# Optimization experiments

Measured on AMD Instinct MI355X. Metric: run time of the kernel, lower is better.

Reference implementation:

```python
import jax, jax.numpy as jnp
import numpy as np

H, W = 256, 256          # resolution from __init__ default
FLOW_SCALING = 256.0     # max(resolution)
MAX_TS = 1.0             # events timestamps normalized to [0, 1]
EPS = 1e-9


def _warp_event(events, flow, tref, ts_weights=None):
    """Bilinear splatting of motion-compensated events into per-polarity IWE.
    events: [B,N,4] (ts,x,y,p); flow: [B,N,2]. Returns [B,2,H,W]."""
    ts = events[..., 0]                      # [B,N]
    x = events[..., 1]
    y = events[..., 2]
    pol = events[..., 3]
    # warped (floating-point) positions
    wx = x + (tref - ts) * flow[..., 0] * FLOW_SCALING
    wy = y + (tref - ts) * flow[..., 1] * FLOW_SCALING
    lx = jnp.floor(wx)
    ty = jnp.floor(wy)
    # 4 bilinear corners: [B,4,N]
    cx = jnp.stack([lx, lx + 1.0, lx, lx + 1.0], axis=1)
    cy = jnp.stack([ty, ty, ty + 1.0, ty + 1.0], axis=1)
    w = (jnp.maximum(0.0, 1.0 - jnp.abs(wx[:, None, :] - cx))
         * jnp.maximum(0.0, 1.0 - jnp.abs(wy[:, None, :] - cy)))
    inb = (cx >= 0) & (cx <= W - 1) & (cy >= 0) & (cy <= H - 1)
    w = jnp.where(inb, w, 0.0)
    if ts_weights is not None:               # optional per-event weight (ts)
        w = w * ts_weights[:, None, :]
    flat = (jnp.clip(cy, 0, H - 1) * W + jnp.clip(cx, 0, W - 1)).astype(jnp.int32)

    def splat(f, ww):  # scatter-add one batch element into flat H*W histogram
        return jnp.zeros(H * W, dtype=w.dtype).at[f.reshape(-1)].add(ww.reshape(-1))

    pos_w = jnp.where((pol == 1)[:, None, :], w, 0.0)
    neg_w = jnp.where((pol == -1)[:, None, :], w, 0.0)
    iwe_pos = jax.vmap(splat)(flat, pos_w).reshape(-1, H, W)
    iwe_neg = jax.vmap(splat)(flat, neg_w).reshape(-1, H, W)
    return jnp.stack([iwe_pos, iwe_neg], axis=1)  # [B,2,H,W]


def _warp_contrast(tref, flow, events):
    iwe = _warp_event(events, flow, tref)
    ts_iwe = _warp_event(events, flow, tref, ts_weights=events[..., 0])
    ts_iwe = ts_iwe / (iwe + EPS)
    loss = (ts_iwe ** 2).sum(axis=(1, 2, 3))           # [B]
    non_zero = ((iwe[:, 0] + iwe[:, 1]) > 0).astype(iwe.dtype)
    return loss / non_zero.sum(axis=(1, 2))


def setup_inputs() -> dict:
    key = jax.random.key(0)
    k1, k2, k3, k4, k5 = jax.random.split(key, 5)
    B, N = 2, 1_000_000
    ts = jax.random.uniform(k1, (B, N))
    x = jax.random.uniform(k2, (B, N)) * (W - 1)
    y = jax.random.uniform(k3, (B, N)) * (H - 1)
    p = jnp.where(jax.random.bernoulli(k4, 0.5, (B, N)), 1.0, -1.0)
    events = jnp.stack([ts, x, y, p], axis=-1).astype(jnp.float32)  # [B,N,4]
    flow = (jax.random.normal(k5, (B, N, 2)) * 0.05).astype(jnp.float32)
    return {"events": events, "flow": flow}


def reference(events, flow):
    # temporal contrast-maximization loss: forward + backward warp per pass
    fw = _warp_contrast(MAX_TS, flow, events).sum() / MAX_TS ** 2
    bw = _warp_contrast(0.0, flow, events).sum() / MAX_TS ** 2
    return fw + bw
```

## Files before the change

### kernel.cpp

```cpp
#include <hip/hip_runtime.h>

#define HH 256
#define WW 256
#define HW (HH * WW)
#define BATCH 2
#define NPASS 2
#define EPSF 1e-9f
#define FLOW_SCALE 256.0f

#define NBLK1 512
#define NCH 4
#define SCAP 1280
#define CAP 4288
#define FPSCALE 16777216.0f
#define FPINV (1.0f / 16777216.0f)

__global__ __launch_bounds__(256) void ew_bin8(
    const float4* __restrict__ events, const float2* __restrict__ flow,
    float* __restrict__ recs, unsigned* __restrict__ tbl, int N) {
  const int b = blockIdx.y;
  const int gblk = b * NBLK1 + blockIdx.x;
  events += (size_t)b * N;
  flow += (size_t)b * N;
  const int EB = (N + NBLK1 - 1) / NBLK1;
  const int i0 = blockIdx.x * EB;
  const int iend = (i0 + EB < N) ? i0 + EB : N;
  const int CEB = (EB + NCH - 1) / NCH;

  __shared__ float stage[SCAP * 3];
  __shared__ unsigned cnt[128], scan[128], start[128], cur[128];
  __shared__ unsigned s_base;
  if (threadIdx.x == 0) s_base = 0u;

  float* __restrict__ myrecs = recs + (size_t)gblk * CAP * 3;

  for (int c = 0; c < NCH; ++c) {
    const int j0 = i0 + c * CEB;
    int j1 = j0 + CEB;
    if (j1 > iend) j1 = iend;
    if (threadIdx.x < 128) {
      cnt[threadIdx.x] = 0u;
      cur[threadIdx.x] = 0u;
    }
    __syncthreads();

    for (int i = j0 + threadIdx.x; i < j1; i += 256) {
      const float4 e = events[i];
      const float2 f = flow[i];
#pragma unroll
      for (int pass = 0; pass < 2; ++pass) {
        const float tref = (pass == 0) ? 1.0f : 0.0f;
        const float dt = tref - e.x;
        const float wx = fmaf(dt * f.x, FLOW_SCALE, e.y);
        const float wy = fmaf(dt * f.y, FLOW_SCALE, e.z);
        const int lx = (int)floorf(wx), ly = (int)floorf(wy);
        int txs[2], tys[2], nx = 0, ny = 0;
        if ((unsigned)lx < 256u) txs[nx++] = lx >> 5;
        if ((unsigned)(lx + 1) < 256u &&
            (lx < 0 || (((lx + 1) >> 5) != (lx >> 5))))
          txs[nx++] = (lx + 1) >> 5;
        if ((unsigned)ly < 256u) tys[ny++] = ly >> 5;
        if ((unsigned)(ly + 1) < 256u &&
            (ly < 0 || (((ly + 1) >> 5) != (ly >> 5))))
          tys[ny++] = (ly + 1) >> 5;
        for (int a = 0; a < ny; ++a)
          for (int c2 = 0; c2 < nx; ++c2)
            atomicAdd(&cnt[pass * 64 + tys[a] * 8 + txs[c2]], 1u);
      }
    }
    __syncthreads();

    if (threadIdx.x < 64) {
      const int l = threadIdx.x;
      unsigned a = cnt[l], bq = cnt[64 + l];
      for (int off = 1; off < 64; off <<= 1) {
        const unsigned ta = __shfl_up(a, off, 64);
        const unsigned tb = __shfl_up(bq, off, 64);
        if (l >= off) {
          a += ta;
          bq += tb;
        }
      }
      const unsigned tot0 = __shfl(a, 63, 64);
      scan[l] = a;
      scan[64 + l] = bq + tot0;
    }
    __syncthreads();

    const unsigned base = s_base;
    unsigned total = scan[127];
    if (total > SCAP) total = SCAP;
    if (total > CAP - base) total = CAP - base;
    if (threadIdx.x < 128) {
      const unsigned c0 = cnt[threadIdx.x];
      const unsigned st = scan[threadIdx.x] - c0;
      unsigned ec = 0u;
      if (st < total) ec = (c0 < total - st) ? c0 : (total - st);
      start[threadIdx.x] = st;
      tbl[((size_t)gblk * 128 + threadIdx.x) * NCH + c] =
          (base + st) | (ec << 16);
    }
    __syncthreads();

    for (int i = j0 + threadIdx.x; i < j1; i += 256) {
      const float4 e = events[i];
      const float2 f = flow[i];
      const float tsp = copysignf(e.x, e.w);
#pragma unroll
      for (int pass = 0; pass < 2; ++pass) {
        const float tref = (pass == 0) ? 1.0f : 0.0f;
        const float dt = tref - e.x;
        const float wx = fmaf(dt * f.x, FLOW_SCALE, e.y);
        const float wy = fmaf(dt * f.y, FLOW_SCALE, e.z);
        const int lx = (int)floorf(wx), ly = (int)floorf(wy);
        int txs[2], tys[2], nx = 0, ny = 0;
        if ((unsigned)lx < 256u) txs[nx++] = lx >> 5;
        if ((unsigned)(lx + 1) < 256u &&
            (lx < 0 || (((lx + 1) >> 5) != (lx >> 5))))
          txs[nx++] = (lx + 1) >> 5;
        if ((unsigned)ly < 256u) tys[ny++] = ly >> 5;
        if ((unsigned)(ly + 1) < 256u &&
            (ly < 0 || (((ly + 1) >> 5) != (ly >> 5))))
          tys[ny++] = (ly + 1) >> 5;
        for (int a = 0; a < ny; ++a)
          for (int c2 = 0; c2 < nx; ++c2) {
            const int bin = pass * 64 + tys[a] * 8 + txs[c2];
            const unsigned pos = start[bin] + atomicAdd(&cur[bin], 1u);
            if (pos < total) {
              stage[pos * 3 + 0] = wx;
              stage[pos * 3 + 1] = wy;
              stage[pos * 3 + 2] = tsp;
            }
          }
      }
    }
    __syncthreads();

    const unsigned nf = total * 3;
    float* __restrict__ dst = myrecs + (size_t)base * 3;
    for (unsigned j = threadIdx.x; j < nf; j += 256) dst[j] = stage[j];
    __syncthreads();
    if (threadIdx.x == 0) s_base = base + total;
  }
}

__global__ __launch_bounds__(512) void ew_accum9(
    const float* __restrict__ recs, const uint4* __restrict__ tbl4,
    unsigned long long* __restrict__ histU, int nrep) {
  const int gbin = blockIdx.x;
  const int rep = blockIdx.y;
  const int b = gbin >> 7;
  const int bin127 = gbin & 127;
  const int pass = (gbin >> 6) & 1;
  const int tile = gbin & 63;
  const int tx0 = (tile & 7) * 32;
  const int ty0 = (tile >> 3) * 32;
  const int pb = pass * 2 + b;

  __shared__ unsigned long long lds64[2048];
  for (int j = threadIdx.x; j < 2048; j += 512) lds64[j] = 0ull;
  __syncthreads();

  const int bpr = NBLK1 / nrep;
  const int blk0 = rep * bpr;
  const int grp = threadIdx.x >> 3;
  const int lane = threadIdx.x & 7;
  for (int r = blk0 + grp; r < blk0 + bpr; r += 64) {
    const int gblk = b * NBLK1 + r;
    const float* __restrict__ blkrec = recs + (size_t)gblk * CAP * 3;
    const uint4 tv = tbl4[(size_t)gblk * 128 + bin127];
    const unsigned tvs[4] = {tv.x, tv.y, tv.z, tv.w};
#pragma unroll
    for (int c = 0; c < NCH; ++c) {
      const unsigned st = tvs[c] & 0xffffu;
      const unsigned ct = tvs[c] >> 16;
      for (unsigned k = lane; k < ct; k += 8) {
        const float wx = blkrec[(st + k) * 3 + 0];
        const float wy = blkrec[(st + k) * 3 + 1];
        const unsigned tb = __float_as_uint(blkrec[(st + k) * 3 + 2]);
        const int spol = (int)(tb >> 31);
        const float ts = __uint_as_float(tb & 0x7fffffffu);
        const int lx = (int)floorf(wx), ly = (int)floorf(wy);
        const float fx = wx - (float)lx;
        const float fy = wy - (float)ly;
        const float wxs[2] = {1.0f - fx, fx};
        const float wys[2] = {1.0f - fy, fy};
#pragma unroll
        for (int dy = 0; dy < 2; ++dy) {
          const int lcy = ly + dy - ty0;
          if ((unsigned)lcy >= 32u) continue;
#pragma unroll
          for (int dx = 0; dx < 2; ++dx) {
            const int lcx = lx + dx - tx0;
            if ((unsigned)lcx >= 32u) continue;
            const float w = wxs[dx] * wys[dy];
            const unsigned wq = __float2uint_rn(w * FPSCALE);
            const unsigned tq = __float2uint_rn(w * ts * FPSCALE);
            const unsigned long long v =
                ((unsigned long long)wq << 32) | (unsigned long long)tq;
            atomicAdd(&lds64[spol * 1024 + lcy * 32 + lcx], v);
          }
        }
      }
    }
  }
  __syncthreads();

  for (int j = threadIdx.x; j < 2048; j += 512) {
    const int spol = j >> 10;
    const int within = j & 1023;
    const size_t px = (size_t)(ty0 + (within >> 5)) * WW + tx0 + (within & 31);
    histU[(((size_t)rep * 4 + pb) * 2 + spol) * HW + px] = lds64[j];
  }
}

__global__ __launch_bounds__(256) void ew_reduce6(
    const unsigned long long* __restrict__ histU, float* __restrict__ partial,
    int nrep) {
  const int sub = blockIdx.x;
  const int pb = blockIdx.y;
  float loss = 0.0f, nz = 0.0f;
  for (int k = threadIdx.x; k < 2048; k += 256) {
    const int pix = sub * 2048 + k;
    unsigned long long v0 = 0ull, v1 = 0ull;
    for (int r = 0; r < nrep; ++r) {
      v0 += histU[(((size_t)r * 4 + pb) * 2 + 0) * HW + pix];
      v1 += histU[(((size_t)r * 4 + pb) * 2 + 1) * HW + pix];
    }
    const float ip = (float)(unsigned)(v0 >> 32) * FPINV;
    const float tp = (float)(unsigned)(v0 & 0xffffffffull) * FPINV;
    const float in_ = (float)(unsigned)(v1 >> 32) * FPINV;
    const float tn = (float)(unsigned)(v1 & 0xffffffffull) * FPINV;
    const float a = tp / (ip + EPSF);
    const float d = tn / (in_ + EPSF);
    loss += a * a + d * d;
    nz += ((ip + in_) > 0.0f) ? 1.0f : 0.0f;
  }
  for (int off = 32; off > 0; off >>= 1) {
    loss += __shfl_down(loss, off, 64);
    nz += __shfl_down(nz, off, 64);
  }
  __shared__ float sl[4], sn[4];
  const int wid = threadIdx.x >> 6;
  if ((threadIdx.x & 63) == 0) {
    sl[wid] = loss;
    sn[wid] = nz;
  }
  __syncthreads();
  if (threadIdx.x == 0) {
    partial[pb * 32 + sub] = sl[0] + sl[1] + sl[2] + sl[3];
    partial[128 + pb * 32 + sub] = sn[0] + sn[1] + sn[2] + sn[3];
  }
}

__global__ void ew_final2(const float* __restrict__ partial,
                          float* __restrict__ out) {
  if (threadIdx.x == 0 && blockIdx.x == 0) {
    float s = 0.0f;
    for (int pb = 0; pb < 4; ++pb) {
      float L = 0.0f, Z = 0.0f;
      for (int j = 0; j < 32; ++j) {
        L += partial[pb * 32 + j];
        Z += partial[128 + pb * 32 + j];
      }
      s += L / Z;
    }
    out[0] = s;
  }
}

#define CHUNKS 8
#define TILES 16
#define TILE_PX 4096
#define REP_FLOATS (CHUNKS * 16 * HW)

__global__ __launch_bounds__(256) void ew_tile(
    const float4* __restrict__ events, const float2* __restrict__ flow,
    float* __restrict__ rep, int N) {
  const int c = blockIdx.x;
  const int tile = blockIdx.y;
  const int pb = blockIdx.z;
  const int b = pb & 1;
  const float tref = (pb >> 1) == 0 ? 1.0f : 0.0f;
  const int tx0 = (tile & 3) * 64;
  const int ty0 = (tile >> 2) * 64;

  __shared__ float lds[4 * TILE_PX];
  for (int j = threadIdx.x; j < 4 * TILE_PX; j += 256) lds[j] = 0.0f;
  __syncthreads();

  events += (size_t)b * N;
  flow += (size_t)b * N;
  const int Nc = (N + CHUNKS - 1) / CHUNKS;
  const int i0 = c * Nc;
  const int i1 = (i0 + Nc < N) ? (i0 + Nc) : N;

  for (int i = i0 + threadIdx.x; i < i1; i += 256) {
    const float4 e = events[i];
    const float2 f = flow[i];
    const float ts = e.x;
    const int pol = (e.w > 0.0f) ? 0 : 1;
    const float dt = tref - ts;
    const float wx = fmaf(dt * f.x, FLOW_SCALE, e.y);
    const float wy = fmaf(dt * f.y, FLOW_SCALE, e.z);
    const float lxf = floorf(wx);
    const float tyf = floorf(wy);
    const float fx = wx - lxf;
    const float fy = wy - tyf;
    const int lx = (int)lxf - tx0;
    const int ty = (int)tyf - ty0;
    const float wxs[2] = {1.0f - fx, fx};
    const float wys[2] = {1.0f - fy, fy};
#pragma unroll
    for (int dy = 0; dy < 2; ++dy) {
      const int cy = ty + dy;
      if ((unsigned)cy >= 64u) continue;
#pragma unroll
      for (int dx = 0; dx < 2; ++dx) {
        const int cx = lx + dx;
        if ((unsigned)cx >= 64u) continue;
        const float w = wxs[dx] * wys[dy];
        const int li = cy * 64 + cx;
        atomicAdd(&lds[pol * TILE_PX + li], w);
        atomicAdd(&lds[(pol + 2) * TILE_PX + li], w * ts);
      }
    }
  }
  __syncthreads();

  float* __restrict__ dst = rep + ((size_t)c * 16 + (size_t)pb * 4) * HW;
  for (int j = threadIdx.x; j < 4 * TILE_PX; j += 256) {
    const int slice = j >> 12;
    const int within = j & (TILE_PX - 1);
    dst[(size_t)slice * HW + (ty0 + (within >> 6)) * WW + tx0 + (within & 63)] =
        lds[j];
  }
}

__global__ __launch_bounds__(256) void ew_reduce2(const float* __restrict__ rep,
                                                  float* __restrict__ partial) {
  const int sub = blockIdx.x;
  const int pb = blockIdx.y;
  float loss = 0.0f, nz = 0.0f;
  for (int k = threadIdx.x; k < 2048; k += 256) {
    const int pix = sub * 2048 + k;
    float ip = 0.0f, in_ = 0.0f, tp = 0.0f, tn = 0.0f;
#pragma unroll
    for (int c = 0; c < CHUNKS; ++c) {
      const float* __restrict__ rb =
          rep + ((size_t)c * 16 + (size_t)pb * 4) * HW + pix;
      ip += rb[0];
      in_ += rb[HW];
      tp += rb[2 * HW];
      tn += rb[3 * HW];
    }
    const float a = tp / (ip + EPSF);
    const float d = tn / (in_ + EPSF);
    loss += a * a + d * d;
    nz += ((ip + in_) > 0.0f) ? 1.0f : 0.0f;
  }
  for (int off = 32; off > 0; off >>= 1) {
    loss += __shfl_down(loss, off, 64);
    nz += __shfl_down(nz, off, 64);
  }
  __shared__ float sl[4], sn[4];
  const int wid = threadIdx.x >> 6;
  if ((threadIdx.x & 63) == 0) {
    sl[wid] = loss;
    sn[wid] = nz;
  }
  __syncthreads();
  if (threadIdx.x == 0) {
    partial[pb * 32 + sub] = sl[0] + sl[1] + sl[2] + sl[3];
    partial[128 + pb * 32 + sub] = sn[0] + sn[1] + sn[2] + sn[3];
  }
}

#define HIST_FLOATS (NPASS * BATCH * 4 * HW)

__global__ __launch_bounds__(256) void ew_scatter(
    const float4* __restrict__ events, const float2* __restrict__ flow,
    float* __restrict__ hist, int N) {
  const int b = blockIdx.y;
  events += (size_t)b * N;
  flow += (size_t)b * N;
  float* __restrict__ hb = hist + (size_t)b * 4 * HW;
  for (int i = blockIdx.x * blockDim.x + threadIdx.x; i < N;
       i += gridDim.x * blockDim.x) {
    const float4 e = events[i];
    const float2 f = flow[i];
    const float ts = e.x, x = e.y, y = e.z, p = e.w;
    const int polofs = (p > 0.0f) ? 0 : HW;
#pragma unroll
    for (int pass = 0; pass < NPASS; ++pass) {
      const float tref = (pass == 0) ? 1.0f : 0.0f;
      const float dt = tref - ts;
      const float wx = fmaf(dt * f.x, FLOW_SCALE, x);
      const float wy = fmaf(dt * f.y, FLOW_SCALE, y);
      const float lxf = floorf(wx), tyf = floorf(wy);
      const float fx = wx - lxf, fy = wy - tyf;
      const int lx = (int)lxf, ty = (int)tyf;
      float* __restrict__ wbase = hb + (size_t)pass * BATCH * 4 * HW + polofs;
      float* __restrict__ tbase = wbase + 2 * HW;
      const float w00 = (1.0f - fx) * (1.0f - fy);
      const float w10 = fx * (1.0f - fy);
      const float w01 = (1.0f - fx) * fy;
      const float w11 = fx * fy;
      const int cx0 = lx, cx1 = lx + 1, cy0 = ty, cy1 = ty + 1;
      const bool inx0 = (cx0 >= 0) & (cx0 < WW);
      const bool inx1 = (cx1 >= 0) & (cx1 < WW);
      const bool iny0 = (cy0 >= 0) & (cy0 < HH);
      const bool iny1 = (cy1 >= 0) & (cy1 < HH);
      if (inx0 & iny0) {
        const int pix = cy0 * WW + cx0;
        atomicAdd(wbase + pix, w00);
        atomicAdd(tbase + pix, w00 * ts);
      }
      if (inx1 & iny0) {
        const int pix = cy0 * WW + cx1;
        atomicAdd(wbase + pix, w10);
        atomicAdd(tbase + pix, w10 * ts);
      }
      if (inx0 & iny1) {
        const int pix = cy1 * WW + cx0;
        atomicAdd(wbase + pix, w01);
        atomicAdd(tbase + pix, w01 * ts);
      }
      if (inx1 & iny1) {
        const int pix = cy1 * WW + cx1;
        atomicAdd(wbase + pix, w11);
        atomicAdd(tbase + pix, w11 * ts);
      }
    }
  }
}

__global__ __launch_bounds__(256) void ew_reduce(const float* __restrict__ hist,
                                                 float* __restrict__ partial) {
  const int g = blockIdx.x;
  const float* __restrict__ base = hist + (size_t)g * 4 * HW;
  double loss = 0.0, nz = 0.0;
  for (int pix = threadIdx.x; pix < HW; pix += blockDim.x) {
    const float ip = base[pix];
    const float in_ = base[HW + pix];
    const float tp = base[2 * HW + pix];
    const float tn = base[3 * HW + pix];
    const float a = tp / (ip + EPSF);
    const float c = tn / (in_ + EPSF);
    loss += (double)(a * a) + (double)(c * c);
    if ((ip + in_) > 0.0f) nz += 1.0;
  }
  for (int off = 32; off > 0; off >>= 1) {
    loss += __shfl_down(loss, off, 64);
    nz += __shfl_down(nz, off, 64);
  }
  __shared__ double sl[4], sn[4];
  const int wid = threadIdx.x >> 6;
  if ((threadIdx.x & 63) == 0) {
    sl[wid] = loss;
    sn[wid] = nz;
  }
  __syncthreads();
  if (threadIdx.x == 0) {
    partial[g] = (float)(sl[0] + sl[1] + sl[2] + sl[3]);
    partial[4 + g] = (float)(sn[0] + sn[1] + sn[2] + sn[3]);
  }
}

__global__ void ew_final(const float* __restrict__ partial,
                         float* __restrict__ out) {
  if (threadIdx.x == 0 && blockIdx.x == 0) {
    float s = 0.0f;
    for (int g = 0; g < NPASS * BATCH; ++g) s += partial[g] / partial[4 + g];
    out[0] = s;
  }
}

extern "C" void kernel_launch(void* const* d_in, const int* in_sizes, int n_in,
                              void* d_out, int out_size, void* d_ws,
                              size_t ws_size, hipStream_t stream) {
  const float4* events = (const float4*)d_in[0];
  const float2* flow = (const float2*)d_in[1];
  float* out = (float*)d_out;
  const int N = in_sizes[0] / (4 * BATCH);

  const size_t recs_bytes = (size_t)BATCH * NBLK1 * CAP * 12;
  const size_t tbl_bytes = (size_t)BATCH * NBLK1 * 128 * NCH * sizeof(unsigned);
  const size_t histU1 = (size_t)4 * 2 * HW * sizeof(unsigned long long);
  const size_t tail = 256 * sizeof(float);
  const size_t need1 = recs_bytes + tbl_bytes + histU1 + tail;
  const size_t need2 = recs_bytes + tbl_bytes + 2 * histU1 + tail;
  const size_t need_tile = ((size_t)REP_FLOATS + 256) * sizeof(float);

  if (ws_size >= need1) {
    const int nrep = (ws_size >= need2) ? 2 : 1;
    float* recs = (float*)d_ws;
    unsigned* tbl = (unsigned*)((char*)d_ws + recs_bytes);
    unsigned long long* histU = (unsigned long long*)((char*)tbl + tbl_bytes);
    float* partial = (float*)((char*)histU + (size_t)nrep * histU1);

    dim3 bgrid(NBLK1, BATCH);
    ew_bin8<<<bgrid, 256, 0, stream>>>(events, flow, recs, tbl, N);
    dim3 agrid(256, nrep);
    ew_accum9<<<agrid, 512, 0, stream>>>(recs, (const uint4*)tbl, histU, nrep);
    dim3 rgrid(32, 4);
    ew_reduce6<<<rgrid, 256, 0, stream>>>(histU, partial, nrep);
    ew_final2<<<1, 64, 0, stream>>>(partial, out);
  } else if (ws_size >= need_tile) {
    float* rep = (float*)d_ws;
    float* partial = rep + REP_FLOATS;
    dim3 tgrid(CHUNKS, TILES, NPASS * BATCH);
    ew_tile<<<tgrid, 256, 0, stream>>>(events, flow, rep, N);
    dim3 rgrid(32, 4);
    ew_reduce2<<<rgrid, 256, 0, stream>>>(rep, partial);
    ew_final2<<<1, 64, 0, stream>>>(partial, out);
  } else {
    float* hist = (float*)d_ws;
    float* partial = hist + HIST_FLOATS;
    hipMemsetAsync(hist, 0, (size_t)HIST_FLOATS * sizeof(float), stream);
    dim3 sgrid(1024, BATCH);
    ew_scatter<<<sgrid, 256, 0, stream>>>(events, flow, hist, N);
    ew_reduce<<<NPASS * BATCH, 256, 0, stream>>>(hist, partial);
    ew_final<<<1, 64, 0, stream>>>(partial, out);
  }
}
```

Before: 76.10 us.

## Cache warped event coordinates in registers between count and scatter phases

The binning kernel now uses twice as many blocks and half as many chunks, so each chunk spans at most two events per thread. Each thread keeps those events' warped coordinates and signed timestamps in registers from the counting phase and reuses them in the scatter phase. This avoids re-reading events and flow from global memory and recomputing the warp. The per-block table, record capacity and reduce grid are resized to match. The accumulate kernel now walks more, smaller per-block segments. The register path silently assumes each chunk has no more than 512 events, which holds only for event counts up to about one million.

```diff
diff --git a/kernel.cpp b/kernel.cpp
--- a/kernel.cpp
+++ b/kernel.cpp
@@ -8,14 +8,14 @@
 #define EPSF 1e-9f
 #define FLOW_SCALE 256.0f
 
-#define NBLK1 512
-#define NCH 4
+#define NBLK1 1024
+#define NCH 2
 #define SCAP 1280
-#define CAP 4288
+#define CAP 2144
 #define FPSCALE 16777216.0f
 #define FPINV (1.0f / 16777216.0f)
 
-__global__ __launch_bounds__(256) void ew_bin8(
+__global__ __launch_bounds__(256) void ew_bin9(
     const float4* __restrict__ events, const float2* __restrict__ flow,
     float* __restrict__ recs, unsigned* __restrict__ tbl, int N) {
   const int b = blockIdx.y;
@@ -44,28 +44,36 @@
     }
     __syncthreads();
 
-    for (int i = j0 + threadIdx.x; i < j1; i += 256) {
-      const float4 e = events[i];
-      const float2 f = flow[i];
-#pragma unroll
-      for (int pass = 0; pass < 2; ++pass) {
-        const float tref = (pass == 0) ? 1.0f : 0.0f;
-        const float dt = tref - e.x;
-        const float wx = fmaf(dt * f.x, FLOW_SCALE, e.y);
-        const float wy = fmaf(dt * f.y, FLOW_SCALE, e.z);
-        const int lx = (int)floorf(wx), ly = (int)floorf(wy);
-        int txs[2], tys[2], nx = 0, ny = 0;
-        if ((unsigned)lx < 256u) txs[nx++] = lx >> 5;
-        if ((unsigned)(lx + 1) < 256u &&
-            (lx < 0 || (((lx + 1) >> 5) != (lx >> 5))))
-          txs[nx++] = (lx + 1) >> 5;
-        if ((unsigned)ly < 256u) tys[ny++] = ly >> 5;
-        if ((unsigned)(ly + 1) < 256u &&
-            (ly < 0 || (((ly + 1) >> 5) != (ly >> 5))))
-          tys[ny++] = (ly + 1) >> 5;
-        for (int a = 0; a < ny; ++a)
-          for (int c2 = 0; c2 < nx; ++c2)
-            atomicAdd(&cnt[pass * 64 + tys[a] * 8 + txs[c2]], 1u);
+    float rwx[2][2], rwy[2][2], rtsp[2];
+#pragma unroll
+    for (int s = 0; s < 2; ++s) {
+      const int i = j0 + s * 256 + (int)threadIdx.x;
+      if (i < j1) {
+        const float4 e = events[i];
+        const float2 f = flow[i];
+        rtsp[s] = copysignf(e.x, e.w);
+#pragma unroll
+        for (int pass = 0; pass < 2; ++pass) {
+          const float tref = (pass == 0) ? 1.0f : 0.0f;
+          const float dt = tref - e.x;
+          const float wx = fmaf(dt * f.x, FLOW_SCALE, e.y);
+          const float wy = fmaf(dt * f.y, FLOW_SCALE, e.z);
+          rwx[s][pass] = wx;
+          rwy[s][pass] = wy;
+          const int lx = (int)floorf(wx), ly = (int)floorf(wy);
+          int txs[2], tys[2], nx = 0, ny = 0;
+          if ((unsigned)lx < 256u) txs[nx++] = lx >> 5;
+          if ((unsigned)(lx + 1) < 256u &&
+              (lx < 0 || (((lx + 1) >> 5) != (lx >> 5))))
+            txs[nx++] = (lx + 1) >> 5;
+          if ((unsigned)ly < 256u) tys[ny++] = ly >> 5;
+          if ((unsigned)(ly + 1) < 256u &&
+              (ly < 0 || (((ly + 1) >> 5) != (ly >> 5))))
+            tys[ny++] = (ly + 1) >> 5;
+          for (int a = 0; a < ny; ++a)
+            for (int c2 = 0; c2 < nx; ++c2)
+              atomicAdd(&cnt[pass * 64 + tys[a] * 8 + txs[c2]], 1u);
+        }
       }
     }
     __syncthreads();
@@ -102,36 +110,36 @@
     }
     __syncthreads();
 
-    for (int i = j0 + threadIdx.x; i < j1; i += 256) {
-      const float4 e = events[i];
-      const float2 f = flow[i];
-      const float tsp = copysignf(e.x, e.w);
-#pragma unroll
-      for (int pass = 0; pass < 2; ++pass) {
-        const float tref = (pass == 0) ? 1.0f : 0.0f;
-        const float dt = tref - e.x;
-        const float wx = fmaf(dt * f.x, FLOW_SCALE, e.y);
-        const float wy = fmaf(dt * f.y, FLOW_SCALE, e.z);
-        const int lx = (int)floorf(wx), ly = (int)floorf(wy);
-        int txs[2], tys[2], nx = 0, ny = 0;
-        if ((unsigned)lx < 256u) txs[nx++] = lx >> 5;
-        if ((unsigned)(lx + 1) < 256u &&
-            (lx < 0 || (((lx + 1) >> 5) != (lx >> 5))))
-          txs[nx++] = (lx + 1) >> 5;
-        if ((unsigned)ly < 256u) tys[ny++] = ly >> 5;
-        if ((unsigned)(ly + 1) < 256u &&
-            (ly < 0 || (((ly + 1) >> 5) != (ly >> 5))))
-          tys[ny++] = (ly + 1) >> 5;
-        for (int a = 0; a < ny; ++a)
-          for (int c2 = 0; c2 < nx; ++c2) {
-            const int bin = pass * 64 + tys[a] * 8 + txs[c2];
-            const unsigned pos = start[bin] + atomicAdd(&cur[bin], 1u);
-            if (pos < total) {
-              stage[pos * 3 + 0] = wx;
-              stage[pos * 3 + 1] = wy;
-              stage[pos * 3 + 2] = tsp;
+#pragma unroll
+    for (int s = 0; s < 2; ++s) {
+      const int i = j0 + s * 256 + (int)threadIdx.x;
+      if (i < j1) {
+        const float tsp = rtsp[s];
+#pragma unroll
+        for (int pass = 0; pass < 2; ++pass) {
+          const float wx = rwx[s][pass];
+          const float wy = rwy[s][pass];
+          const int lx = (int)floorf(wx), ly = (int)floorf(wy);
+          int txs[2], tys[2], nx = 0, ny = 0;
+          if ((unsigned)lx < 256u) txs[nx++] = lx >> 5;
+          if ((unsigned)(lx + 1) < 256u &&
+              (lx < 0 || (((lx + 1) >> 5) != (lx >> 5))))
+            txs[nx++] = (lx + 1) >> 5;
+          if ((unsigned)ly < 256u) tys[ny++] = ly >> 5;
+          if ((unsigned)(ly + 1) < 256u &&
+              (ly < 0 || (((ly + 1) >> 5) != (ly >> 5))))
+            tys[ny++] = (ly + 1) >> 5;
+          for (int a = 0; a < ny; ++a)
+            for (int c2 = 0; c2 < nx; ++c2) {
+              const int bin = pass * 64 + tys[a] * 8 + txs[c2];
+              const unsigned pos = start[bin] + atomicAdd(&cur[bin], 1u);
+              if (pos < total) {
+                stage[pos * 3 + 0] = wx;
+                stage[pos * 3 + 1] = wy;
+                stage[pos * 3 + 2] = tsp;
+              }
             }
-          }
+        }
       }
     }
     __syncthreads();
@@ -144,8 +152,8 @@
   }
 }
 
-__global__ __launch_bounds__(512) void ew_accum9(
-    const float* __restrict__ recs, const uint4* __restrict__ tbl4,
+__global__ __launch_bounds__(512) void ew_accum10(
+    const float* __restrict__ recs, const uint2* __restrict__ tbl2,
     unsigned long long* __restrict__ histU, int nrep) {
   const int gbin = blockIdx.x;
   const int rep = blockIdx.y;
@@ -168,8 +176,8 @@
   for (int r = blk0 + grp; r < blk0 + bpr; r += 64) {
     const int gblk = b * NBLK1 + r;
     const float* __restrict__ blkrec = recs + (size_t)gblk * CAP * 3;
-    const uint4 tv = tbl4[(size_t)gblk * 128 + bin127];
-    const unsigned tvs[4] = {tv.x, tv.y, tv.z, tv.w};
+    const uint2 tv = tbl2[(size_t)gblk * 128 + bin127];
+    const unsigned tvs[2] = {tv.x, tv.y};
 #pragma unroll
     for (int c = 0; c < NCH; ++c) {
       const unsigned st = tvs[c] & 0xffffu;
@@ -214,14 +222,14 @@
   }
 }
 
-__global__ __launch_bounds__(256) void ew_reduce6(
+__global__ __launch_bounds__(256) void ew_reduce7(
     const unsigned long long* __restrict__ histU, float* __restrict__ partial,
     int nrep) {
   const int sub = blockIdx.x;
   const int pb = blockIdx.y;
   float loss = 0.0f, nz = 0.0f;
-  for (int k = threadIdx.x; k < 2048; k += 256) {
-    const int pix = sub * 2048 + k;
+  for (int k = threadIdx.x; k < 1024; k += 256) {
+    const int pix = sub * 1024 + k;
     unsigned long long v0 = 0ull, v1 = 0ull;
     for (int r = 0; r < nrep; ++r) {
       v0 += histU[(((size_t)r * 4 + pb) * 2 + 0) * HW + pix];
@@ -248,20 +256,20 @@
   }
   __syncthreads();
   if (threadIdx.x == 0) {
-    partial[pb * 32 + sub] = sl[0] + sl[1] + sl[2] + sl[3];
-    partial[128 + pb * 32 + sub] = sn[0] + sn[1] + sn[2] + sn[3];
-  }
-}
-
-__global__ void ew_final2(const float* __restrict__ partial,
+    partial[pb * 64 + sub] = sl[0] + sl[1] + sl[2] + sl[3];
+    partial[256 + pb * 64 + sub] = sn[0] + sn[1] + sn[2] + sn[3];
+  }
+}
+
+__global__ void ew_final3(const float* __restrict__ partial,
                           float* __restrict__ out) {
   if (threadIdx.x == 0 && blockIdx.x == 0) {
     float s = 0.0f;
     for (int pb = 0; pb < 4; ++pb) {
       float L = 0.0f, Z = 0.0f;
-      for (int j = 0; j < 32; ++j) {
-        L += partial[pb * 32 + j];
-        Z += partial[128 + pb * 32 + j];
+      for (int j = 0; j < 64; ++j) {
+        L += partial[pb * 64 + j];
+        Z += partial[256 + pb * 64 + j];
       }
       s += L / Z;
     }
@@ -373,6 +381,22 @@
   if (threadIdx.x == 0) {
     partial[pb * 32 + sub] = sl[0] + sl[1] + sl[2] + sl[3];
     partial[128 + pb * 32 + sub] = sn[0] + sn[1] + sn[2] + sn[3];
+  }
+}
+
+__global__ void ew_final2(const float* __restrict__ partial,
+                          float* __restrict__ out) {
+  if (threadIdx.x == 0 && blockIdx.x == 0) {
+    float s = 0.0f;
+    for (int pb = 0; pb < 4; ++pb) {
+      float L = 0.0f, Z = 0.0f;
+      for (int j = 0; j < 32; ++j) {
+        L += partial[pb * 32 + j];
+        Z += partial[128 + pb * 32 + j];
+      }
+      s += L / Z;
+    }
+    out[0] = s;
   }
 }
 
@@ -487,7 +511,7 @@
   const size_t recs_bytes = (size_t)BATCH * NBLK1 * CAP * 12;
   const size_t tbl_bytes = (size_t)BATCH * NBLK1 * 128 * NCH * sizeof(unsigned);
   const size_t histU1 = (size_t)4 * 2 * HW * sizeof(unsigned long long);
-  const size_t tail = 256 * sizeof(float);
+  const size_t tail = 512 * sizeof(float);
   const size_t need1 = recs_bytes + tbl_bytes + histU1 + tail;
   const size_t need2 = recs_bytes + tbl_bytes + 2 * histU1 + tail;
   const size_t need_tile = ((size_t)REP_FLOATS + 256) * sizeof(float);
@@ -500,12 +524,12 @@
     float* partial = (float*)((char*)histU + (size_t)nrep * histU1);
 
     dim3 bgrid(NBLK1, BATCH);
-    ew_bin8<<<bgrid, 256, 0, stream>>>(events, flow, recs, tbl, N);
+    ew_bin9<<<bgrid, 256, 0, stream>>>(events, flow, recs, tbl, N);
     dim3 agrid(256, nrep);
-    ew_accum9<<<agrid, 512, 0, stream>>>(recs, (const uint4*)tbl, histU, nrep);
-    dim3 rgrid(32, 4);
-    ew_reduce6<<<rgrid, 256, 0, stream>>>(histU, partial, nrep);
-    ew_final2<<<1, 64, 0, stream>>>(partial, out);
+    ew_accum10<<<agrid, 512, 0, stream>>>(recs, (const uint2*)tbl, histU, nrep);
+    dim3 rgrid(64, 4);
+    ew_reduce7<<<rgrid, 256, 0, stream>>>(histU, partial, nrep);
+    ew_final3<<<1, 64, 0, stream>>>(partial, out);
   } else if (ws_size >= need_tile) {
     float* rep = (float*)d_ws;
     float* partial = rep + REP_FLOATS;
```

Result: faster. 68.78 us (-9.6%).
